# Kernel optimization log

Hardware: AMD Instinct MI355X
Metric: run time of the kernel (lower is better)

Reference implementation:

```python
import jax, jax.numpy as jnp
import numpy as np
import math

D_MODEL = 256
SIGMA = 1.0


def _sinusoidal_pe(L, d_model, dtype=jnp.float32):
    # pe[l, 2i] = sin(l * w_i), pe[l, 2i+1] = cos(l * w_i)
    position = jnp.arange(L, dtype=dtype)[:, None]                       # [L,1]
    div_term = jnp.exp(jnp.arange(0, d_model, 2, dtype=dtype) * (-math.log(10000.0) / d_model))
    pe = jnp.zeros((L, d_model), dtype=dtype)
    pe = pe.at[:, 0::2].set(jnp.sin(position * div_term))
    pe = pe.at[:, 1::2].set(jnp.cos(position * div_term))
    return pe  # [L, d_model]


def setup_inputs() -> dict:
    key = jax.random.key(0)
    # scale 0.05 keeps pairwise sq-distances O(1) so S = exp(-d/2) is non-degenerate
    x = jax.random.normal(key, (4, 4096, 256), dtype=jnp.float32) * 0.05
    return {"x": x}


def reference(x):
    B, L, D = x.shape
    pe = _sinusoidal_pe(L, D_MODEL, dtype=x.dtype)[None]                 # [1,L,D]
    # pairwise squared distances via the expansion ||a||^2+||b||^2-2ab (avoids [B,L,L,D])
    sq = jnp.sum(x * x, axis=-1)                                         # [B,L]
    gram = jnp.einsum('bld,bmd->blm', x, x)                              # [B,L,L]
    dist_sq = jnp.maximum(sq[:, :, None] + sq[:, None, :] - 2.0 * gram, 0.0)
    S = jnp.exp(-dist_sq / (2.0 * SIGMA ** 2))                           # [B,L,L]
    sem = jnp.einsum('blm,bmd->bld', S, x) / jnp.sum(S, axis=-1, keepdims=True)
    return x + pe + sem
```

## Files before the change

kernel.cpp:

```cpp
#include <hip/hip_runtime.h>

typedef unsigned char u8;
typedef float f32x4 __attribute__((ext_vector_type(4)));
typedef float f32x16 __attribute__((ext_vector_type(16)));
typedef int i32x8 __attribute__((ext_vector_type(8)));

#define LL 4096
#define PSTR 136
#define SCALE 16.0f
#define GSCALE (1.0f/256.0f)
#define FREQC (-0.03597789207803197f)
#define ONE_SC 0x7F7F7F7F

__device__ __forceinline__ long LCAST(uint2 v) { return __builtin_bit_cast(long, v); }
__device__ __forceinline__ i32x8 PK8(uint2 a, uint2 b, uint2 c, uint2 d) {
  i32x8 r;
  r[0] = (int)a.x; r[1] = (int)a.y; r[2] = (int)b.x; r[3] = (int)b.y;
  r[4] = (int)c.x; r[5] = (int)c.y; r[6] = (int)d.x; r[7] = (int)d.y;
  return r;
}

typedef __attribute__((address_space(3))) u8 lds_u8;
typedef __attribute__((address_space(1))) u8 glb_u8;
__device__ __forceinline__ void dma16(const u8* g, u8* l) {
  __builtin_amdgcn_global_load_lds((const glb_u8*)g, (lds_u8*)l, 16, 0, 0);
}

__global__ __launch_bounds__(512) void prep2(const float* __restrict__ x, u8* __restrict__ xbf,
                                             u8* __restrict__ xT, float* __restrict__ sq) {
  __shared__ u8 T2[256 * 72];
  const int blk = blockIdx.x;
  const int b = blk >> 6, ch = blk & 63;
  const int j0 = ch << 6;
  const int tid = threadIdx.x;
  const int wv = tid >> 6, ln = tid & 63;
  const long bL = (long)b * LL;
  const float4* x4 = (const float4*)x + (bL + j0) * 64;
  unsigned* xb4 = (unsigned*)xbf + (bL + j0) * 64;

  #pragma unroll
  for (int g = 0; g < 2; ++g) {
    int pkw[4];
    #pragma unroll
    for (int ii = 0; ii < 4; ++ii) {
      const int row = 8 * wv + 4 * g + ii;
      float4 v = x4[row * 64 + ln];
      float s = v.x * v.x + v.y * v.y + v.z * v.z + v.w * v.w;
      #pragma unroll
      for (int o = 32; o; o >>= 1) s += __shfl_xor(s, o);
      if (ln == 0) sq[bL + j0 + row] = s;
      int pk = __builtin_amdgcn_cvt_pk_fp8_f32(v.x * SCALE, v.y * SCALE, 0, false);
      pk = __builtin_amdgcn_cvt_pk_fp8_f32(v.z * SCALE, v.w * SCALE, pk, true);
      const int sdw = (((ln >> 1) ^ ((j0 + row) & 31)) << 1) | (ln & 1);
      xb4[row * 64 + sdw] = (unsigned)pk;
      pkw[ii] = pk;
    }
    const int rb = 8 * wv + 4 * g;
    #pragma unroll
    for (int k = 0; k < 4; ++k) {
      const unsigned sel = (unsigned)(k | ((4 + k) << 8));
      unsigned m01 = __builtin_amdgcn_perm((unsigned)pkw[1], (unsigned)pkw[0], sel);
      unsigned m23 = __builtin_amdgcn_perm((unsigned)pkw[3], (unsigned)pkw[2], sel);
      unsigned tw  = __builtin_amdgcn_perm(m23, m01, 0x05040100u);
      *(unsigned*)(T2 + (4 * ln + k) * 72 + rb) = tw;
    }
  }
  __syncthreads();
  #pragma unroll
  for (int db = 0; db < 2; ++db) {
    const int d = db * 128 + (tid >> 2);
    const int oct2 = tid & 3;
    const int key = d & 15;
    const int hb = ((ch & 1) << 3) ^ (key & 8);
    const int p0 = hb + 2 * oct2;
    const int c0 = (p0 ^ key) & 7;
    const int c1 = ((p0 + 1) ^ key) & 7;
    uint2 lo = *(const uint2*)(T2 + d * 72 + 8 * c0);
    uint2 hi = *(const uint2*)(T2 + d * 72 + 8 * c1);
    uint4 ov; ov.x = lo.x; ov.y = lo.y; ov.z = hi.x; ov.w = hi.y;
    *(uint4*)(xT + (((long)(b << 8) + d) << 12) + ((ch >> 1) << 7) + (hb << 3) + (oct2 << 4)) = ov;
  }
}

__global__ __launch_bounds__(512, 2) void tpe_main(
    const u8* __restrict__ xbf, const u8* __restrict__ xT,
    const float* __restrict__ sqv,
    const float* __restrict__ x, float* __restrict__ out) {
  __shared__ u8 Kt[2][32768];
  __shared__ u8 Ps[2][64 * PSTR];
  __shared__ float lred[8][64];
  __shared__ float linv[64];

  const int tid = threadIdx.x;
  const int w = tid >> 6;
  const int lane = tid & 63;
  const int l15 = lane & 15, l31 = lane & 31;
  const int q4 = lane >> 4;
  const int q2 = lane >> 5;

  const int blk = blockIdx.x;
  const int b = (blk & 7) >> 1;
  const int qt = ((blk >> 3) << 1) | (blk & 1);
  const int q0 = qt << 6;
  const long bL = (long)b * LL;

  i32x8 qmx[4][2];
  float qa[4];
  #pragma unroll
  for (int t = 0; t < 4; ++t) {
    const int row = q0 + 16 * t + l15;
    const u8* qrow = xbf + ((bL + row) << 8);
    const int key = row & 31;
    #pragma unroll
    for (int u = 0; u < 2; ++u) {
      const int cb = 16 * u + 4 * q4;
      uint2 c0 = *(const uint2*)(qrow + (((cb + 0) ^ key) << 3));
      uint2 c1 = *(const uint2*)(qrow + (((cb + 1) ^ key) << 3));
      uint2 c2 = *(const uint2*)(qrow + (((cb + 2) ^ key) << 3));
      uint2 c3 = *(const uint2*)(qrow + (((cb + 3) ^ key) << 3));
      qmx[t][u] = PK8(c0, c1, c2, c3);
    }
    qa[t] = -0.5f * sqv[bL + row];
  }

  f32x16 oacc[2];
  #pragma unroll
  for (int rb = 0; rb < 2; ++rb)
    #pragma unroll
    for (int k = 0; k < 16; ++k) oacc[rb][k] = 0.f;
  float rsacc[4] = {0.f, 0.f, 0.f, 0.f};

  const u8* kbat = xbf + (bL << 8);
  const u8* vseg = xT + (((long)(b << 8) + 32 * w + l31) << 12);
  const int vkey = l31 & 15;

  i32x8 vfA[2], vfB[2];

  #pragma unroll
  for (int c = 0; c < 4; ++c) {
    int off = c * 8192 + tid * 16;
    dma16(kbat + off, Kt[0] + off);
  }
  __syncthreads();

#define TPE_ITER(IT, KCUR, KNXT, PPREV, PCUR, VFC, VFN)                                     \
  {                                                                                         \
    const int j0 = (IT) << 7;                                                               \
    if ((IT) < 31) {    \
      const u8* ks = kbat + ((long)((IT) + 1) << 15);                                       \
      _Pragma("unroll")                                                                     \
      for (int c = 0; c < 4; ++c) {                                                         \
        int off = c * 8192 + tid * 16;                                                      \
        dma16(ks + off, (KNXT) + off);                                                      \
      }                                                                                     \
    }                                                                                       \
    float4 skv4 = *(const float4*)(sqv + bL + j0 + 16 * w + 4 * q4);                        \
    if ((IT) != 0) {   \
      _Pragma("unroll")                                                                     \
      for (int u = 0; u < 2; ++u) {                                                         \
        const u8* pr0 = (PPREV) + l31 * PSTR + 64 * u + 32 * q2;                            \
        const u8* pr1 = pr0 + 32 * PSTR;                                                    \
        i32x8 pa0 = PK8(*(const uint2*)(pr0),      *(const uint2*)(pr0 + 8),                \
                        *(const uint2*)(pr0 + 16), *(const uint2*)(pr0 + 24));              \
        i32x8 pa1 = PK8(*(const uint2*)(pr1),      *(const uint2*)(pr1 + 8),                \
                        *(const uint2*)(pr1 + 16), *(const uint2*)(pr1 + 24));              \
        oacc[0] = __builtin_amdgcn_mfma_scale_f32_32x32x64_f8f6f4(                          \
            pa0, VFC[u], oacc[0], 0, 0, 0, ONE_SC, 0, ONE_SC);                              \
        oacc[1] = __builtin_amdgcn_mfma_scale_f32_32x32x64_f8f6f4(                          \
            pa1, VFC[u], oacc[1], 0, 0, 0, ONE_SC, 0, ONE_SC);                              \
      }                                                                                     \
    }                                                                                       \
    _Pragma("unroll") \
    for (int u = 0; u < 2; ++u) {                                                           \
      const int cb = 8 * u + 4 * q2;                                                        \
      uint2 v0 = *(const uint2*)(vseg + j0 + (((cb + 0) ^ vkey) << 3));                     \
      uint2 v1 = *(const uint2*)(vseg + j0 + (((cb + 1) ^ vkey) << 3));                     \
      uint2 v2 = *(const uint2*)(vseg + j0 + (((cb + 2) ^ vkey) << 3));                     \
      uint2 v3 = *(const uint2*)(vseg + j0 + (((cb + 3) ^ vkey) << 3));                     \
      VFN[u] = PK8(v0, v1, v2, v3);                                                         \
    }                                                                                       \
    {                            \
      const int krow = 16 * w + l15;                                                        \
      const int kkey = krow & 31;                                                           \
      const u8* kb2 = (KCUR) + krow * 256;                                                  \
      f32x4 sacc[4];                                                                        \
      _Pragma("unroll")                                                                     \
      for (int t = 0; t < 4; ++t) {                                                         \
        sacc[t][0] = 0.f; sacc[t][1] = 0.f; sacc[t][2] = 0.f; sacc[t][3] = 0.f;             \
      }                                                                                     \
      _Pragma("unroll")                                                                     \
      for (int u = 0; u < 2; ++u) {                                                         \
        const int cb = 16 * u + 4 * q4;                                                     \
        uint2 k0 = *(const uint2*)(kb2 + (((cb + 0) ^ kkey) << 3));                         \
        uint2 k1 = *(const uint2*)(kb2 + (((cb + 1) ^ kkey) << 3));                         \
        uint2 k2 = *(const uint2*)(kb2 + (((cb + 2) ^ kkey) << 3));                         \
        uint2 k3 = *(const uint2*)(kb2 + (((cb + 3) ^ kkey) << 3));                         \
        i32x8 af = PK8(k0, k1, k2, k3);                                                     \
        _Pragma("unroll")                                                                   \
        for (int t = 0; t < 4; ++t)                                                         \
          sacc[t] = __builtin_amdgcn_mfma_scale_f32_16x16x128_f8f6f4(                       \
              af, qmx[t][u], sacc[t], 0, 0, 0, ONE_SC, 0, ONE_SC);                          \
      }                                                                                     \
      _Pragma("unroll")        \
      for (int t = 0; t < 4; ++t) {                 \
        float p0 = __expf(fminf(fmaf(sacc[t][0], GSCALE, qa[t] + skv4.x), 0.f));            \
        float p1 = __expf(fminf(fmaf(sacc[t][1], GSCALE, qa[t] + skv4.y), 0.f));            \
        float p2 = __expf(fminf(fmaf(sacc[t][2], GSCALE, qa[t] + skv4.z), 0.f));            \
        float p3 = __expf(fminf(fmaf(sacc[t][3], GSCALE, qa[t] + skv4.w), 0.f));            \
        rsacc[t] += (p0 + p1) + (p2 + p3);                                                  \
        int pk = __builtin_amdgcn_cvt_pk_fp8_f32(p0, p1, 0, false);                         \
        pk = __builtin_amdgcn_cvt_pk_fp8_f32(p2, p3, pk, true);                             \
        *(int*)((PCUR) + (16 * t + l15) * PSTR + 16 * w + 4 * q4) = pk;                     \
      }                                                                                     \
    }                                                                                       \
    __syncthreads();         \
  }

  for (int it2 = 0; it2 < 16; ++it2) {
    TPE_ITER(2 * it2,     Kt[0], Kt[1], Ps[1], Ps[0], vfA, vfB)
    TPE_ITER(2 * it2 + 1, Kt[1], Kt[0], Ps[0], Ps[1], vfB, vfA)
  }
#undef TPE_ITER

  #pragma unroll
  for (int u = 0; u < 2; ++u) {
    const u8* pr0 = Ps[1] + l31 * PSTR + 64 * u + 32 * q2;
    const u8* pr1 = pr0 + 32 * PSTR;
    i32x8 pa0 = PK8(*(const uint2*)(pr0),      *(const uint2*)(pr0 + 8),
                    *(const uint2*)(pr0 + 16), *(const uint2*)(pr0 + 24));
    i32x8 pa1 = PK8(*(const uint2*)(pr1),      *(const uint2*)(pr1 + 8),
                    *(const uint2*)(pr1 + 16), *(const uint2*)(pr1 + 24));
    oacc[0] = __builtin_amdgcn_mfma_scale_f32_32x32x64_f8f6f4(
        pa0, vfA[u], oacc[0], 0, 0, 0, ONE_SC, 0, ONE_SC);
    oacc[1] = __builtin_amdgcn_mfma_scale_f32_32x32x64_f8f6f4(
        pa1, vfA[u], oacc[1], 0, 0, 0, ONE_SC, 0, ONE_SC);
  }

  #pragma unroll
  for (int t = 0; t < 4; ++t) {
    float r = rsacc[t];
    r += __shfl_xor(r, 16);
    r += __shfl_xor(r, 32);
    if (lane < 16) lred[w][16 * t + l15] = r;
  }
  __syncthreads();
  if (tid < 64) {
    float s = 0.f;
    #pragma unroll
    for (int ww = 0; ww < 8; ++ww) s += lred[ww][tid];
    linv[tid] = 0.0625f / s;
  }
  __syncthreads();
  const int col = 32 * w + l31;
  const float freq = __expf((float)(col & ~1) * FREQC);
  #pragma unroll
  for (int rb = 0; rb < 2; ++rb) {
    #pragma unroll
    for (int reg = 0; reg < 16; ++reg) {
      int row = 32 * rb + 4 * q2 + (reg & 3) + 8 * (reg >> 2);
      int l = q0 + row;
      float ang = (float)l * freq;
      float pv = (col & 1) ? __cosf(ang) : __sinf(ang);
      long off = ((bL + l) << 8) + col;
      out[off] = oacc[rb][reg] * linv[row] + x[off] + pv;
    }
  }
}

extern "C" void kernel_launch(void* const* d_in, const int* in_sizes, int n_in,
                              void* d_out, int out_size, void* d_ws, size_t ws_size,
                              hipStream_t stream) {
  const float* x = (const float*)d_in[0];
  float* out = (float*)d_out;
  char* ws = (char*)d_ws;
  u8* xbf = (u8*)ws;
  u8* xT = (u8*)(ws + 4194304);
  float* sq = (float*)(ws + 8388608);
  prep2<<<256, 512, 0, stream>>>(x, xbf, xT, sq);
  tpe_main<<<256, 512, 0, stream>>>(xbf, xT, sq, x, out);
}
```

Measured before the change: 152.3 us.

## Switch fp8 operand swizzle to 16-byte granularity for wider LDS/global loads

Changes the XOR swizzle of the fp8 copies of x (row-major and transposed) from 8-byte to 16-byte chunks, so the Q, K, V and P fragments load with uint4 reads instead of uint2. The P buffer stride goes from 136 to 144 and the prep kernel's transpose staging stride from 72 to 80, keeping 16-byte alignment. The aim is to halve the number of LDS and global load instructions feeding the MFMAs. In exchange, bank-conflict behaviour changes with the new swizzle and strides, and each block uses a little more shared memory.

```diff
diff --git a/kernel.cpp b/kernel.cpp
--- a/kernel.cpp
+++ b/kernel.cpp
@@ -6,17 +6,16 @@
 typedef int i32x8 __attribute__((ext_vector_type(8)));
 
 #define LL 4096
-#define PSTR 136
+#define PSTR 144
 #define SCALE 16.0f
 #define GSCALE (1.0f/256.0f)
 #define FREQC (-0.03597789207803197f)
 #define ONE_SC 0x7F7F7F7F
 
-__device__ __forceinline__ long LCAST(uint2 v) { return __builtin_bit_cast(long, v); }
-__device__ __forceinline__ i32x8 PK8(uint2 a, uint2 b, uint2 c, uint2 d) {
+__device__ __forceinline__ i32x8 PK16(uint4 a, uint4 b) {
   i32x8 r;
-  r[0] = (int)a.x; r[1] = (int)a.y; r[2] = (int)b.x; r[3] = (int)b.y;
-  r[4] = (int)c.x; r[5] = (int)c.y; r[6] = (int)d.x; r[7] = (int)d.y;
+  r[0] = (int)a.x; r[1] = (int)a.y; r[2] = (int)a.z; r[3] = (int)a.w;
+  r[4] = (int)b.x; r[5] = (int)b.y; r[6] = (int)b.z; r[7] = (int)b.w;
   return r;
 }
 
@@ -26,9 +25,9 @@
   __builtin_amdgcn_global_load_lds((const glb_u8*)g, (lds_u8*)l, 16, 0, 0);
 }
 
-__global__ __launch_bounds__(512) void prep2(const float* __restrict__ x, u8* __restrict__ xbf,
+__global__ __launch_bounds__(512) void prep3(const float* __restrict__ x, u8* __restrict__ xbf,
                                              u8* __restrict__ xT, float* __restrict__ sq) {
-  __shared__ u8 T2[256 * 72];
+  __shared__ u8 T2[256 * 80];
   const int blk = blockIdx.x;
   const int b = blk >> 6, ch = blk & 63;
   const int j0 = ch << 6;
@@ -51,7 +50,7 @@
       if (ln == 0) sq[bL + j0 + row] = s;
       int pk = __builtin_amdgcn_cvt_pk_fp8_f32(v.x * SCALE, v.y * SCALE, 0, false);
       pk = __builtin_amdgcn_cvt_pk_fp8_f32(v.z * SCALE, v.w * SCALE, pk, true);
-      const int sdw = (((ln >> 1) ^ ((j0 + row) & 31)) << 1) | (ln & 1);
+      const int sdw = ((((ln >> 2) ^ ((j0 + row) & 15)) << 2)) | (ln & 3);
       xb4[row * 64 + sdw] = (unsigned)pk;
       pkw[ii] = pk;
     }
@@ -62,23 +61,18 @@
       unsigned m01 = __builtin_amdgcn_perm((unsigned)pkw[1], (unsigned)pkw[0], sel);
       unsigned m23 = __builtin_amdgcn_perm((unsigned)pkw[3], (unsigned)pkw[2], sel);
       unsigned tw  = __builtin_amdgcn_perm(m23, m01, 0x05040100u);
-      *(unsigned*)(T2 + (4 * ln + k) * 72 + rb) = tw;
+      *(unsigned*)(T2 + (4 * ln + k) * 80 + rb) = tw;
     }
   }
   __syncthreads();
   #pragma unroll
   for (int db = 0; db < 2; ++db) {
     const int d = db * 128 + (tid >> 2);
-    const int oct2 = tid & 3;
-    const int key = d & 15;
-    const int hb = ((ch & 1) << 3) ^ (key & 8);
-    const int p0 = hb + 2 * oct2;
-    const int c0 = (p0 ^ key) & 7;
-    const int c1 = ((p0 + 1) ^ key) & 7;
-    uint2 lo = *(const uint2*)(T2 + d * 72 + 8 * c0);
-    uint2 hi = *(const uint2*)(T2 + d * 72 + 8 * c1);
-    uint4 ov; ov.x = lo.x; ov.y = lo.y; ov.z = hi.x; ov.w = hi.y;
-    *(uint4*)(xT + (((long)(b << 8) + d) << 12) + ((ch >> 1) << 7) + (hb << 3) + (oct2 << 4)) = ov;
+    const int cl = tid & 3;
+    const int c16 = ((ch & 1) << 2) | cl;
+    const int p = c16 ^ (d & 7);
+    uint4 ov = *(const uint4*)(T2 + d * 80 + 16 * cl);
+    *(uint4*)(xT + (((long)(b << 8) + d) << 12) + ((ch >> 1) << 7) + (p << 4)) = ov;
   }
 }
 
@@ -86,8 +80,8 @@
     const u8* __restrict__ xbf, const u8* __restrict__ xT,
     const float* __restrict__ sqv,
     const float* __restrict__ x, float* __restrict__ out) {
-  __shared__ u8 Kt[2][32768];
-  __shared__ u8 Ps[2][64 * PSTR];
+  __shared__ __align__(16) u8 Kt[2][32768];
+  __shared__ __align__(16) u8 Ps[2][64 * PSTR];
   __shared__ float lred[8][64];
   __shared__ float linv[64];
 
@@ -110,15 +104,12 @@
   for (int t = 0; t < 4; ++t) {
     const int row = q0 + 16 * t + l15;
     const u8* qrow = xbf + ((bL + row) << 8);
-    const int key = row & 31;
     #pragma unroll
     for (int u = 0; u < 2; ++u) {
-      const int cb = 16 * u + 4 * q4;
-      uint2 c0 = *(const uint2*)(qrow + (((cb + 0) ^ key) << 3));
-      uint2 c1 = *(const uint2*)(qrow + (((cb + 1) ^ key) << 3));
-      uint2 c2 = *(const uint2*)(qrow + (((cb + 2) ^ key) << 3));
-      uint2 c3 = *(const uint2*)(qrow + (((cb + 3) ^ key) << 3));
-      qmx[t][u] = PK8(c0, c1, c2, c3);
+      const int cb = 8 * u + 2 * q4;
+      uint4 lo = *(const uint4*)(qrow + (((cb + 0) ^ l15) << 4));
+      uint4 hi = *(const uint4*)(qrow + (((cb + 1) ^ l15) << 4));
+      qmx[t][u] = PK16(lo, hi);
     }
     qa[t] = -0.5f * sqv[bL + row];
   }
@@ -132,7 +123,7 @@
 
   const u8* kbat = xbf + (bL << 8);
   const u8* vseg = xT + (((long)(b << 8) + 32 * w + l31) << 12);
-  const int vkey = l31 & 15;
+  const int vk7 = l31 & 7;
 
   i32x8 vfA[2], vfB[2];
 
@@ -155,33 +146,28 @@
       }                                                                                     \
     }                                                                                       \
     float4 skv4 = *(const float4*)(sqv + bL + j0 + 16 * w + 4 * q4);                        \
-    if ((IT) != 0) {   \
+    if ((IT) != 0) {  \
       _Pragma("unroll")                                                                     \
       for (int u = 0; u < 2; ++u) {                                                         \
         const u8* pr0 = (PPREV) + l31 * PSTR + 64 * u + 32 * q2;                            \
-        const u8* pr1 = pr0 + 32 * PSTR;                                                    \
-        i32x8 pa0 = PK8(*(const uint2*)(pr0),      *(const uint2*)(pr0 + 8),                \
-                        *(const uint2*)(pr0 + 16), *(const uint2*)(pr0 + 24));              \
-        i32x8 pa1 = PK8(*(const uint2*)(pr1),      *(const uint2*)(pr1 + 8),                \
-                        *(const uint2*)(pr1 + 16), *(const uint2*)(pr1 + 24));              \
+        i32x8 pa0 = PK16(*(const uint4*)(pr0), *(const uint4*)(pr0 + 16));                  \
+        i32x8 pa1 = PK16(*(const uint4*)(pr0 + 32 * PSTR),                                  \
+                         *(const uint4*)(pr0 + 32 * PSTR + 16));                            \
         oacc[0] = __builtin_amdgcn_mfma_scale_f32_32x32x64_f8f6f4(                          \
             pa0, VFC[u], oacc[0], 0, 0, 0, ONE_SC, 0, ONE_SC);                              \
         oacc[1] = __builtin_amdgcn_mfma_scale_f32_32x32x64_f8f6f4(                          \
             pa1, VFC[u], oacc[1], 0, 0, 0, ONE_SC, 0, ONE_SC);                              \
       }                                                                                     \
     }                                                                                       \
-    _Pragma("unroll") \
+    _Pragma("unroll")              \
     for (int u = 0; u < 2; ++u) {                                                           \
-      const int cb = 8 * u + 4 * q2;                                                        \
-      uint2 v0 = *(const uint2*)(vseg + j0 + (((cb + 0) ^ vkey) << 3));                     \
-      uint2 v1 = *(const uint2*)(vseg + j0 + (((cb + 1) ^ vkey) << 3));                     \
-      uint2 v2 = *(const uint2*)(vseg + j0 + (((cb + 2) ^ vkey) << 3));                     \
-      uint2 v3 = *(const uint2*)(vseg + j0 + (((cb + 3) ^ vkey) << 3));                     \
-      VFN[u] = PK8(v0, v1, v2, v3);                                                         \
+      const int cb = 4 * u + 2 * q2;                                                        \
+      uint4 v0 = *(const uint4*)(vseg + j0 + (((cb + 0) ^ vk7) << 4));                      \
+      uint4 v1 = *(const uint4*)(vseg + j0 + (((cb + 1) ^ vk7) << 4));                      \
+      VFN[u] = PK16(v0, v1);                                                                \
     }                                                                                       \
     {                            \
       const int krow = 16 * w + l15;                                                        \
-      const int kkey = krow & 31;                                                           \
       const u8* kb2 = (KCUR) + krow * 256;                                                  \
       f32x4 sacc[4];                                                                        \
       _Pragma("unroll")                                                                     \
@@ -190,12 +176,10 @@
       }                                                                                     \
       _Pragma("unroll")                                                                     \
       for (int u = 0; u < 2; ++u) {                                                         \
-        const int cb = 16 * u + 4 * q4;                                                     \
-        uint2 k0 = *(const uint2*)(kb2 + (((cb + 0) ^ kkey) << 3));                         \
-        uint2 k1 = *(const uint2*)(kb2 + (((cb + 1) ^ kkey) << 3));                         \
-        uint2 k2 = *(const uint2*)(kb2 + (((cb + 2) ^ kkey) << 3));                         \
-        uint2 k3 = *(const uint2*)(kb2 + (((cb + 3) ^ kkey) << 3));                         \
-        i32x8 af = PK8(k0, k1, k2, k3);                                                     \
+        const int cb = 8 * u + 2 * q4;                                                      \
+        uint4 klo = *(const uint4*)(kb2 + (((cb + 0) ^ l15) << 4));                         \
+        uint4 khi = *(const uint4*)(kb2 + (((cb + 1) ^ l15) << 4));                         \
+        i32x8 af = PK16(klo, khi);                                                          \
         _Pragma("unroll")                                                                   \
         for (int t = 0; t < 4; ++t)                                                         \
           sacc[t] = __builtin_amdgcn_mfma_scale_f32_16x16x128_f8f6f4(                       \
@@ -225,11 +209,8 @@
   #pragma unroll
   for (int u = 0; u < 2; ++u) {
     const u8* pr0 = Ps[1] + l31 * PSTR + 64 * u + 32 * q2;
-    const u8* pr1 = pr0 + 32 * PSTR;
-    i32x8 pa0 = PK8(*(const uint2*)(pr0),      *(const uint2*)(pr0 + 8),
-                    *(const uint2*)(pr0 + 16), *(const uint2*)(pr0 + 24));
-    i32x8 pa1 = PK8(*(const uint2*)(pr1),      *(const uint2*)(pr1 + 8),
-                    *(const uint2*)(pr1 + 16), *(const uint2*)(pr1 + 24));
+    i32x8 pa0 = PK16(*(const uint4*)(pr0), *(const uint4*)(pr0 + 16));
+    i32x8 pa1 = PK16(*(const uint4*)(pr0 + 32 * PSTR), *(const uint4*)(pr0 + 32 * PSTR + 16));
     oacc[0] = __builtin_amdgcn_mfma_scale_f32_32x32x64_f8f6f4(
         pa0, vfA[u], oacc[0], 0, 0, 0, ONE_SC, 0, ONE_SC);
     oacc[1] = __builtin_amdgcn_mfma_scale_f32_32x32x64_f8f6f4(
@@ -276,6 +257,6 @@
   u8* xbf = (u8*)ws;
   u8* xT = (u8*)(ws + 4194304);
   float* sq = (float*)(ws + 8388608);
-  prep2<<<256, 512, 0, stream>>>(x, xbf, xT, sq);
+  prep3<<<256, 512, 0, stream>>>(x, xbf, xT, sq);
   tpe_main<<<256, 512, 0, stream>>>(xbf, xT, sq, x, out);
 }
```

Measured after the change: 123.9 us. 1.23x faster.
